# Kernel tuning notes

Measured on AMD Instinct MI355X. Metric: run time of the kernel, lower is better.

## Reference

```python
import jax, jax.numpy as jnp
import numpy as np

B = 4096
D = 512
N_I = 1000000
N_T = 1000000
GAMMA = 0.8
EPS = 1e-10
RHO_I = 8.0
RHO_T = 8.0
ETA_INIT = 1e-05
BETA_U = 0.5
GRAD_CLIP = 5.0
TAU_MIN, TAU_MAX = 0.005, 0.05
TAU_INIT = 0.01


def setup_inputs() -> dict:
    key = jax.random.key(0)
    k1, k2 = jax.random.split(key)
    img = jax.random.normal(k1, (B, D), jnp.float32)
    txt = jax.random.normal(k2, (B, D), jnp.float32)
    # CLIP-style L2-normalized features
    img = img / jnp.linalg.norm(img, axis=1, keepdims=True)
    txt = txt / jnp.linalg.norm(txt, axis=1, keepdims=True)
    return {
        "image_features": img,
        "text_features": txt,
        "s_I": jnp.zeros(N_I, jnp.float32),
        "s_T": jnp.zeros(N_T, jnp.float32),
        "b_I": jnp.zeros(N_I, jnp.float32),
        "b_T": jnp.zeros(N_T, jnp.float32),
        "u_I": jnp.zeros(N_I, jnp.float32),
        "u_T": jnp.zeros(N_T, jnp.float32),
        "tau_I": jnp.full((N_I,), TAU_INIT, jnp.float32),
        "tau_T": jnp.full((N_T,), TAU_INIT, jnp.float32),
        "image_ids": jnp.arange(B, dtype=jnp.int32),
        "text_ids": jnp.arange(B, dtype=jnp.int32),
        "epoch": 1,
    }


def reference(image_features, text_features, s_I, s_T, b_I, b_T, u_I, u_T,
              tau_I, tau_T, image_ids, text_ids, epoch):
    sg = jax.lax.stop_gradient
    sim = jnp.einsum('id,jd->ij', image_features, text_features)  # [B,B]
    diag = jnp.diagonal(sim)
    Bn = sim.shape[0]
    tau_img = tau_I[image_ids]  # [B]
    tau_txt = tau_T[text_ids]   # [B]
    image_diffs = sim - diag[:, None]
    text_diffs = sim - diag[None, :]
    # .detach() in the original -> stop_gradient here
    idt = sg(image_diffs / tau_img[:, None])
    tdt = sg(text_diffs / tau_txt[None, :])
    old_b_I = b_I[image_ids]
    old_b_T = b_T[text_ids]
    # running max for log-sum-exp stabilization
    b_I_row = jnp.maximum(idt.max(axis=1), old_b_I)
    b_T_col = jnp.maximum(tdt.max(axis=0), old_b_T)
    b_I_new = b_I.at[image_ids].set(b_I_row)
    b_T_new = b_T.at[text_ids].set(b_T_col)
    mask = 1.0 - jnp.eye(Bn, dtype=sim.dtype)
    exp_i = jnp.exp(idt - b_I_row[:, None]) * mask
    exp_t = jnp.exp(tdt - b_T_col[None, :]) * mask
    g_I = exp_i.sum(axis=1)
    g_T = exp_t.sum(axis=0)
    if epoch == 0:
        sI = g_I
        sT = g_T
    else:
        sI = (1.0 - GAMMA) * s_I[image_ids] * jnp.exp(old_b_I - b_I_row) + GAMMA * g_I
        sT = (1.0 - GAMMA) * s_T[text_ids] * jnp.exp(old_b_T - b_T_col) + GAMMA * g_T
    s_I_new = s_I.at[image_ids].set(sI)
    s_T_new = s_T.at[text_ids].set(sT)
    w_i = sg(exp_i / (sI[:, None] + EPS))
    w_t = sg(exp_t / (sT[None, :] + EPS))
    image_loss = (w_i * image_diffs).sum(axis=1)
    text_loss = (w_t * text_diffs).sum(axis=0)
    total_loss = image_loss.mean() + text_loss.mean()
    tw_i = jnp.log(sI / (Bn - 1)) + b_I_row + RHO_I - (w_i * idt).sum(axis=1)
    tw_t = jnp.log(sT / (Bn - 1)) + b_T_col + RHO_T - (w_t * tdt).sum(axis=0)
    # torch uses in-place clamp_ on a view, so the returned means are clipped
    tw_i = jnp.clip(tw_i, -GRAD_CLIP, GRAD_CLIP)
    tw_t = jnp.clip(tw_t, -GRAD_CLIP, GRAD_CLIP)
    u_I_val = (1.0 - BETA_U) * u_I[image_ids] + BETA_U * tw_i
    u_T_val = (1.0 - BETA_U) * u_T[text_ids] + BETA_U * tw_t
    u_I_new = u_I.at[image_ids].set(u_I_val)
    u_T_new = u_T.at[text_ids].set(u_T_val)
    tau_I_new = tau_I.at[image_ids].set(jnp.clip(tau_img - ETA_INIT * u_I_val, TAU_MIN, TAU_MAX))
    tau_T_new = tau_T.at[text_ids].set(jnp.clip(tau_txt - ETA_INIT * u_T_val, TAU_MIN, TAU_MAX))
    return (total_loss, tau_img.mean(), tau_txt.mean(), tw_i.mean(), tw_t.mean(),
            s_I_new, s_T_new, b_I_new, b_T_new, u_I_new, u_T_new, tau_I_new, tau_T_new)
```

## Files before the change

kernel.cpp:

```cpp
#include <hip/hip_runtime.h>

typedef unsigned short u16;
typedef unsigned int u32;

typedef __bf16 bf16x8 __attribute__((ext_vector_type(8)));
typedef float floatx4 __attribute__((ext_vector_type(4)));

__device__ __forceinline__ u16 f2bf(float f) {
    union { float f; u32 u; } c; c.f = f;
    u32 u = c.u;
    u32 r = u + 0x7FFFu + ((u >> 16) & 1u);
    return (u16)(r >> 16);
}
__device__ __forceinline__ float bf2f(u16 x) {
    union { u32 u; float f; } c; c.u = ((u32)x) << 16; return c.f;
}

__device__ __forceinline__ void comb(float& M, float& P0, float& P1,
                                     float m, float p0, float p1) {
    float nm = fmaxf(M, m);
    float s = __expf(M - nm), t = __expf(m - nm);
    P0 = P0 * s + p0 * t;
    P1 = P1 * s + p1 * t;
    M = nm;
}

__device__ __forceinline__ void gload16(const void* g, void* l) {
    __builtin_amdgcn_global_load_lds(
        (const __attribute__((address_space(1))) void*)g,
        (__attribute__((address_space(3))) void*)l, 16, 0, 0);
}

__global__ __launch_bounds__(256) void presplit(
    const float* __restrict__ a, const float* __restrict__ b,
    u16* __restrict__ Ah, u16* __restrict__ Al,
    u16* __restrict__ Bh, u16* __restrict__ Bl, int n,
    const float* __restrict__ tauI, const float* __restrict__ tauT,
    const int* __restrict__ img_ids, const int* __restrict__ txt_ids,
    float* __restrict__ taur, float* __restrict__ tauc,
    u32* __restrict__ ctrl) {
    if (blockIdx.y == 0 && blockIdx.x == 0 && threadIdx.x < 8)
        ctrl[threadIdx.x] = 0u;
    if (blockIdx.y == 0 && blockIdx.x < 16) {
        int t = blockIdx.x * 256 + threadIdx.x;
        taur[t] = tauI[img_ids[t]];
        tauc[t] = tauT[txt_ids[t]];
    }
    const float* src = blockIdx.y ? b : a;
    u16* dh = blockIdx.y ? Bh : Ah;
    u16* dl = blockIdx.y ? Bl : Al;
    int i = (blockIdx.x * 256 + threadIdx.x) * 8;
    if (i >= n) return;
    float4 v0 = *(const float4*)&src[i];
    float4 v1 = *(const float4*)&src[i + 4];
    float xs[8] = {v0.x, v0.y, v0.z, v0.w, v1.x, v1.y, v1.z, v1.w};
    u16 h[8], l[8];
#pragma unroll
    for (int e = 0; e < 8; e++) {
        h[e] = f2bf(xs[e]);
        l[e] = f2bf(xs[e] - bf2f(h[e]));
    }
    int r = i >> 9, k = i & 511;
    int off = (((r >> 4) << 4) + (k >> 5)) * 512 + ((((k >> 3) & 3) << 4) + (r & 15)) * 8;
    *(uint4*)&dh[off] = *(uint4*)h;
    *(uint4*)&dl[off] = *(uint4*)l;
}

__global__ __launch_bounds__(512, 2) void gemm_flash(
    const u16* __restrict__ Ah, const u16* __restrict__ Al,
    const u16* __restrict__ Bh, const u16* __restrict__ Bl,
    const float* __restrict__ taur, const float* __restrict__ tauc,
    float* __restrict__ rowpart, float* __restrict__ colpart,
    float* __restrict__ diag,
    const float* __restrict__ p0, const float* __restrict__ p1,
    const float* __restrict__ p2, const float* __restrict__ p3,
    const float* __restrict__ p4, const float* __restrict__ p5,
    const float* __restrict__ p6, const float* __restrict__ p7,
    float* __restrict__ out, long long n) {
    __shared__ u16 tiles[65536];

    const int bid  = blockIdx.x;
    const int tid  = threadIdx.x;
    const int wave = tid >> 6, lane = tid & 63;
    const int lr = lane & 15, quad = lane >> 4;
    const int waveM = wave >> 2, waveN = wave & 3;
    const int x = bid & 7, s = bid >> 3;
    const int rowtile = (x >> 2) * 8 + (s >> 2);
    const int coltile = (x & 3) * 4 + (s & 3);
    const int rowBase = rowtile * 256;
    const int colBase = coltile * 256;

    const int sa = wave >> 1;
    const u16* gb = (sa == 0) ? Ah : (sa == 1) ? Al : (sa == 2) ? Bh : Bl;
    const int base16 = ((sa < 2) ? rowBase : colBase) >> 4;
    const int jb = (wave & 1) * 8;

#define STAGE(slice, bufb)                                                    \
    {                                                                         \
        _Pragma("unroll")                                                     \
        for (int j = 0; j < 8; j++) {                                         \
            size_t ge = ((size_t)(base16 + jb + j)) * 8192 +                  \
                        (size_t)(slice) * 512 + lane * 8;                     \
            gload16(gb + ge, &tiles[(bufb) + (wave * 8 + j) * 512]);          \
        }                                                                     \
    }

    floatx4 acc[8][4];
#pragma unroll
    for (int mi = 0; mi < 8; mi++)
#pragma unroll
        for (int ni = 0; ni < 4; ni++) acc[mi][ni] = (floatx4)0.0f;

    const int Gq = (int)((n - 3) >> 2);
    const int ni32 = (int)n;
    float* dst5 = out + 5;

    STAGE(0, 0)

    if (bid == 0 && tid < 32) {
        int arr = tid >> 2, j = tid & 3;
        const float* sp = (arr & 4) ? ((arr & 2) ? ((arr & 1) ? p7 : p6) : ((arr & 1) ? p5 : p4))
                                    : ((arr & 2) ? ((arr & 1) ? p3 : p2) : ((arr & 1) ? p1 : p0));
        float* dp = dst5 + (size_t)arr * (size_t)n;
        long long tail0 = 3 + 4 * (long long)Gq;
        if (j < 3) dp[j] = sp[j];
        else
            for (long long z = tail0; z < n; z++) dp[z] = sp[z];
    }
    __syncthreads();

#pragma unroll 1
    for (int t = 0; t < 16; t++) {
        const int cb = (t & 1) << 15;
        const int nb = cb ^ 32768;
        if (t < 15) STAGE(t + 1, nb)

        bool docopy = false;
        float c0 = 0.f, c1 = 0.f, c2 = 0.f, c3 = 0.f;
        int cdst = 0;
        {
            int c = bid * 512 + tid + t * 131072;
            int ck = c >> 18;
            int g = c & 262143;
            if (g < Gq) {
                docopy = true;
                int ce = 3 + 4 * g;
                cdst = ck * ni32 + ce;
                const float* sp = (ck & 4) ? ((ck & 2) ? ((ck & 1) ? p7 : p6) : ((ck & 1) ? p5 : p4))
                                           : ((ck & 2) ? ((ck & 1) ? p3 : p2) : ((ck & 1) ? p1 : p0));
                c0 = sp[ce]; c1 = sp[ce + 1]; c2 = sp[ce + 2]; c3 = sp[ce + 3];
            }
        }

        {
            const int ab = cb + lane * 8;
            bf16x8 bh[4], bl[4];
#pragma unroll
            for (int ni = 0; ni < 4; ni++) {
                bh[ni] = *(const bf16x8*)&tiles[ab + (32 + waveN * 4 + ni) * 512];
                bl[ni] = *(const bf16x8*)&tiles[ab + (48 + waveN * 4 + ni) * 512];
            }
#pragma unroll
            for (int mi = 0; mi < 8; mi++) {
                bf16x8 ah = *(const bf16x8*)&tiles[ab + (waveM * 8 + mi) * 512];
                bf16x8 al = *(const bf16x8*)&tiles[ab + (16 + waveM * 8 + mi) * 512];
#pragma unroll
                for (int ni = 0; ni < 4; ni++) {
                    acc[mi][ni] = __builtin_amdgcn_mfma_f32_16x16x32_bf16(ah, bh[ni], acc[mi][ni], 0, 0, 0);
                    acc[mi][ni] = __builtin_amdgcn_mfma_f32_16x16x32_bf16(ah, bl[ni], acc[mi][ni], 0, 0, 0);
                    acc[mi][ni] = __builtin_amdgcn_mfma_f32_16x16x32_bf16(al, bh[ni], acc[mi][ni], 0, 0, 0);
                }
            }
        }

        if (docopy) {
            float4 q = {c0, c1, c2, c3};
            *(float4*)&dst5[cdst] = q;
        }
        __syncthreads();
    }
#undef STAGE

    float* redbuf = (float*)tiles;

    if (rowtile == coltile) {
#pragma unroll
        for (int mi = 0; mi < 8; mi++)
#pragma unroll
            for (int ni = 0; ni < 4; ni++) {
                if (waveM * 128 + mi * 16 != waveN * 64 + ni * 16) continue;
#pragma unroll
                for (int r = 0; r < 4; r++)
                    if (lr == quad * 4 + r)
                        diag[colBase + waveN * 64 + ni * 16 + lr] = acc[mi][ni][r];
            }
    }

#pragma unroll
    for (int mi = 0; mi < 8; mi++) {
#pragma unroll
        for (int r = 0; r < 4; r++) {
            int row_local = waveM * 128 + mi * 16 + quad * 4 + r;
            float vmax = fmaxf(fmaxf(acc[mi][0][r], acc[mi][1][r]),
                               fmaxf(acc[mi][2][r], acc[mi][3][r]));
#pragma unroll
            for (int mask = 1; mask <= 8; mask <<= 1)
                vmax = fmaxf(vmax, __shfl_xor(vmax, mask));
            float it = 1.0f / taur[rowBase + row_local];
            float M = vmax * it;
            float P0 = 0.f, P1 = 0.f;
#pragma unroll
            for (int ni = 0; ni < 4; ni++) {
                float y = acc[mi][ni][r] * it;
                float e = __expf(y - M);
                P0 += e;
                P1 += y * e;
            }
#pragma unroll
            for (int mask = 1; mask <= 8; mask <<= 1) {
                P0 += __shfl_xor(P0, mask);
                P1 += __shfl_xor(P1, mask);
            }
            if (lr == 0) {
                int xx = (row_local * 4 + waveN) * 3;
                redbuf[xx] = M; redbuf[xx + 1] = P0; redbuf[xx + 2] = P1;
            }
        }
    }

#pragma unroll
    for (int ni = 0; ni < 4; ni++) {
        int col_local = waveN * 64 + ni * 16 + lr;
        float vmax = -3.4e38f;
#pragma unroll
        for (int mi = 0; mi < 8; mi++)
            vmax = fmaxf(vmax,
                fmaxf(fmaxf(acc[mi][ni][0], acc[mi][ni][1]),
                      fmaxf(acc[mi][ni][2], acc[mi][ni][3])));
#pragma unroll
        for (int mask = 16; mask <= 32; mask <<= 1)
            vmax = fmaxf(vmax, __shfl_xor(vmax, mask));
        float it = 1.0f / tauc[colBase + col_local];
        float M = vmax * it;
        float P0 = 0.f, P1 = 0.f;
#pragma unroll
        for (int mi = 0; mi < 8; mi++)
#pragma unroll
            for (int r = 0; r < 4; r++) {
                float y = acc[mi][ni][r] * it;
                float e = __expf(y - M);
                P0 += e;
                P1 += y * e;
            }
#pragma unroll
        for (int mask = 16; mask <= 32; mask <<= 1) {
            P0 += __shfl_xor(P0, mask);
            P1 += __shfl_xor(P1, mask);
        }
        if (quad == 0) {
            int xx = 3072 + (col_local * 2 + waveM) * 3;
            redbuf[xx] = M; redbuf[xx + 1] = P0; redbuf[xx + 2] = P1;
        }
    }
    __syncthreads();

    if (tid < 256) {
        int xx = tid * 12;
        float M = redbuf[xx], P0 = redbuf[xx + 1], P1 = redbuf[xx + 2];
        comb(M, P0, P1, redbuf[xx + 3], redbuf[xx + 4], redbuf[xx + 5]);
        comb(M, P0, P1, redbuf[xx + 6], redbuf[xx + 7], redbuf[xx + 8]);
        comb(M, P0, P1, redbuf[xx + 9], redbuf[xx + 10], redbuf[xx + 11]);
        float* dst = &rowpart[(size_t)(rowBase + tid) * 48 + coltile * 3];
        dst[0] = M; dst[1] = P0; dst[2] = P1;
    } else {
        int c = tid - 256;
        int xx = 3072 + c * 6;
        float M = redbuf[xx], P0 = redbuf[xx + 1], P1 = redbuf[xx + 2];
        comb(M, P0, P1, redbuf[xx + 3], redbuf[xx + 4], redbuf[xx + 5]);
        float* dst = &colpart[(size_t)(colBase + c) * 48 + rowtile * 3];
        dst[0] = M; dst[1] = P0; dst[2] = P1;
    }
}

struct FinArgs {
    const float* rowpart; const float* colpart; const float* diag;
    const float* tauI; const float* sI; const float* bI; const float* uI;
    const float* tauT; const float* sT; const float* bT; const float* uT;
    const int* img_ids; const int* txt_ids; const int* epoch_p;
    float* out; u32* ctrl; long long n;
};

__global__ __launch_bounds__(256) void rows_final(FinArgs a) {
    int t = blockIdx.x * 256 + threadIdx.x;
    int side = t >> 12, i = t & 4095;
    const float* part   = side ? a.colpart : a.rowpart;
    const int*   ids    = side ? a.txt_ids : a.img_ids;
    const float* tau_in = side ? a.tauT : a.tauI;
    const float* s_in   = side ? a.sT   : a.sI;
    const float* b_in   = side ? a.bT   : a.bI;
    const float* u_in   = side ? a.uT   : a.uI;

    const int id = ids[i];
    const float dg = a.diag[i];

    const float4* p4 = (const float4*)(part + (size_t)i * 48);
    float v[48];
#pragma unroll
    for (int k = 0; k < 12; k++) {
        float4 q = p4[k];
        v[4 * k]     = q.x;
        v[4 * k + 1] = q.y;
        v[4 * k + 2] = q.z;
        v[4 * k + 3] = q.w;
    }
    float M = -3.4e38f, P0 = 0.f, P1 = 0.f;
#pragma unroll
    for (int k = 0; k < 16; k++)
        comb(M, P0, P1, v[3 * k], v[3 * k + 1], v[3 * k + 2]);

    const float tau   = tau_in[id];
    const float old_b = b_in[id];
    const float old_s = s_in[id];
    const float old_u = u_in[id];
    const float y_ii  = dg / tau;

    float b_row = fmaxf(M - y_ii, old_b);
    float e  = expf(M - y_ii - b_row);
    float S0 = P0 * e - expf(-b_row);
    float S1 = (P1 - y_ii * P0) * e;

    float g = S0;
    float sI = (*a.epoch_p == 0) ? g
             : 0.2f * old_s * expf(old_b - b_row) + 0.8f * g;
    float denom = sI + 1e-10f;
    float wsum = S1 / denom;
    float lossr = tau * wsum;
    float tw = logf(sI * (1.0f / 4095.0f)) + b_row + 8.0f - wsum;
    tw = fminf(fmaxf(tw, -5.0f), 5.0f);
    float uval = 0.5f * old_u + 0.5f * tw;
    float taun = fminf(fmaxf(tau - 1e-5f * uval, 0.005f), 0.05f);

    float* sect = a.out + 5;
    sect[(size_t)(0 + side) * (size_t)a.n + id] = sI;
    sect[(size_t)(2 + side) * (size_t)a.n + id] = b_row;
    sect[(size_t)(4 + side) * (size_t)a.n + id] = uval;
    sect[(size_t)(6 + side) * (size_t)a.n + id] = taun;

    __shared__ float sred[4][3];
    const int lane = threadIdx.x & 63, wv = threadIdx.x >> 6;
    float r0 = lossr, r1 = tw, r2 = tau;
#pragma unroll
    for (int o = 32; o > 0; o >>= 1) {
        r0 += __shfl_xor(r0, o);
        r1 += __shfl_xor(r1, o);
        r2 += __shfl_xor(r2, o);
    }
    if (lane == 0) { sred[wv][0] = r0; sred[wv][1] = r1; sred[wv][2] = r2; }
    __syncthreads();
    if (threadIdx.x == 0) {
        float t0 = sred[0][0] + sred[1][0] + sred[2][0] + sred[3][0];
        float t1 = sred[0][1] + sred[1][1] + sred[2][1] + sred[3][1];
        float t2 = sred[0][2] + sred[1][2] + sred[2][2] + sred[3][2];
        float* accs = (float*)a.ctrl;
        __hip_atomic_fetch_add(&accs[side * 3 + 0], t0, __ATOMIC_RELAXED,
                               __HIP_MEMORY_SCOPE_AGENT);
        __hip_atomic_fetch_add(&accs[side * 3 + 1], t1, __ATOMIC_RELAXED,
                               __HIP_MEMORY_SCOPE_AGENT);
        __hip_atomic_fetch_add(&accs[side * 3 + 2], t2, __ATOMIC_RELAXED,
                               __HIP_MEMORY_SCOPE_AGENT);
        u32 tk = __hip_atomic_fetch_add(&a.ctrl[6], 1u, __ATOMIC_ACQ_REL,
                                        __HIP_MEMORY_SCOPE_AGENT);
        if (tk == 31u) {
            float s0 = __hip_atomic_fetch_add(&accs[0], 0.0f, __ATOMIC_RELAXED, __HIP_MEMORY_SCOPE_AGENT);
            float s1 = __hip_atomic_fetch_add(&accs[1], 0.0f, __ATOMIC_RELAXED, __HIP_MEMORY_SCOPE_AGENT);
            float s2 = __hip_atomic_fetch_add(&accs[2], 0.0f, __ATOMIC_RELAXED, __HIP_MEMORY_SCOPE_AGENT);
            float s3 = __hip_atomic_fetch_add(&accs[3], 0.0f, __ATOMIC_RELAXED, __HIP_MEMORY_SCOPE_AGENT);
            float s4 = __hip_atomic_fetch_add(&accs[4], 0.0f, __ATOMIC_RELAXED, __HIP_MEMORY_SCOPE_AGENT);
            float s5 = __hip_atomic_fetch_add(&accs[5], 0.0f, __ATOMIC_RELAXED, __HIP_MEMORY_SCOPE_AGENT);
            const float inv = 1.0f / 4096.0f;
            a.out[0] = (s0 + s3) * inv;
            a.out[1] = s2 * inv;
            a.out[2] = s5 * inv;
            a.out[3] = s1 * inv;
            a.out[4] = s4 * inv;
        }
    }
}

extern "C" void kernel_launch(void* const* d_in, const int* in_sizes, int n_in,
                              void* d_out, int out_size, void* d_ws, size_t ws_size,
                              hipStream_t stream) {
    const float* img   = (const float*)d_in[0];
    const float* txt   = (const float*)d_in[1];
    const float* s_I   = (const float*)d_in[2];
    const float* s_T   = (const float*)d_in[3];
    const float* b_I   = (const float*)d_in[4];
    const float* b_T   = (const float*)d_in[5];
    const float* u_I   = (const float*)d_in[6];
    const float* u_T   = (const float*)d_in[7];
    const float* tau_I = (const float*)d_in[8];
    const float* tau_T = (const float*)d_in[9];
    const int* image_ids = (const int*)d_in[10];
    const int* text_ids  = (const int*)d_in[11];
    const int* epoch     = (const int*)d_in[12];
    float* out = (float*)d_out;
    const long long n = in_sizes[2];
    const int nfeat = in_sizes[0];

    const size_t MB = 1024 * 1024;
    u16* Ah = (u16*)d_ws;
    u16* Al = Ah + (size_t)nfeat;
    u16* Bh = Al + (size_t)nfeat;
    u16* Bl = Bh + (size_t)nfeat;
    float* rowpart = (float*)((char*)d_ws + 16 * MB);
    float* colpart = (float*)((char*)d_ws + 18 * MB);
    float* diag    = (float*)((char*)d_ws + 20 * MB);
    float* taur    = (float*)((char*)d_ws + 20 * MB + 256 * 1024);
    float* tauc    = (float*)((char*)d_ws + 20 * MB + 512 * 1024);
    u32*   ctrl    = (u32*)((char*)d_ws + 22 * MB);

    presplit<<<dim3((nfeat / 8 + 255) / 256, 2), 256, 0, stream>>>(
        img, txt, Ah, Al, Bh, Bl, nfeat,
        tau_I, tau_T, image_ids, text_ids, taur, tauc, ctrl);

    gemm_flash<<<256, 512, 0, stream>>>(
        Ah, Al, Bh, Bl, taur, tauc, rowpart, colpart, diag,
        s_I, s_T, b_I, b_T, u_I, u_T, tau_I, tau_T, out, n);

    FinArgs fa;
    fa.rowpart = rowpart; fa.colpart = colpart; fa.diag = diag;
    fa.tauI = tau_I; fa.sI = s_I; fa.bI = b_I; fa.uI = u_I;
    fa.tauT = tau_T; fa.sT = s_T; fa.bT = b_T; fa.uT = u_T;
    fa.img_ids = image_ids; fa.txt_ids = text_ids; fa.epoch_p = epoch;
    fa.out = out; fa.ctrl = ctrl; fa.n = n;
    rows_final<<<32, 256, 0, stream>>>(fa);
}
```

Baseline: 173.1 us.

## Halve GEMM column tile to 128, single-buffer LDS, double grid occupancy

The fused split-bf16 GEMM + flash-style reduction now uses 256x128 output tiles with 512 blocks, a single 48 KB shared buffer instead of a 128 KB double buffer, and launch bounds allowing 4 blocks per CU. The goal is to fill more CUs and raise occupancy so latency is hidden by other resident blocks instead of by explicit double buffering. The parameter-copy work is re-split across the larger grid, and row partials grow from 16 to 32 entries per row, so the final kernel is adjusted to match. Risks: less operand reuse per tile, a sync per K-slice with no prefetch, and possible register spilling under the tighter launch bound.

```diff
diff --git a/kernel.cpp b/kernel.cpp
--- a/kernel.cpp
+++ b/kernel.cpp
@@ -66,7 +66,7 @@
     *(uint4*)&dl[off] = *(uint4*)l;
 }
 
-__global__ __launch_bounds__(512, 2) void gemm_flash(
+__global__ __launch_bounds__(512, 4) void gemm_flash(
     const u16* __restrict__ Ah, const u16* __restrict__ Al,
     const u16* __restrict__ Bh, const u16* __restrict__ Bl,
     const float* __restrict__ taur, const float* __restrict__ tauc,
@@ -77,45 +77,47 @@
     const float* __restrict__ p4, const float* __restrict__ p5,
     const float* __restrict__ p6, const float* __restrict__ p7,
     float* __restrict__ out, long long n) {
-    __shared__ u16 tiles[65536];
+    __shared__ u16 tiles[24576];
 
     const int bid  = blockIdx.x;
     const int tid  = threadIdx.x;
     const int wave = tid >> 6, lane = tid & 63;
     const int lr = lane & 15, quad = lane >> 4;
-    const int waveM = wave >> 2, waveN = wave & 3;
+    const int waveM = wave >> 1, waveN = wave & 1;
     const int x = bid & 7, s = bid >> 3;
-    const int rowtile = (x >> 2) * 8 + (s >> 2);
-    const int coltile = (x & 3) * 4 + (s & 3);
+    const int rowtile = (x >> 2) * 8 + (s >> 3);
+    const int coltile = (x & 3) * 8 + (s & 7);
     const int rowBase = rowtile * 256;
-    const int colBase = coltile * 256;
-
-    const int sa = wave >> 1;
-    const u16* gb = (sa == 0) ? Ah : (sa == 1) ? Al : (sa == 2) ? Bh : Bl;
-    const int base16 = ((sa < 2) ? rowBase : colBase) >> 4;
-    const int jb = (wave & 1) * 8;
-
-#define STAGE(slice, bufb)                                                    \
+    const int colBase = coltile * 128;
+    const int rowBase16 = rowBase >> 4, colBase16 = colBase >> 4;
+    const size_t la = (size_t)(lane * 8);
+
+#define STAGE(slice)                                                          \
     {                                                                         \
-        _Pragma("unroll")                                                     \
-        for (int j = 0; j < 8; j++) {                                         \
-            size_t ge = ((size_t)(base16 + jb + j)) * 8192 +                  \
-                        (size_t)(slice) * 512 + lane * 8;                     \
-            gload16(gb + ge, &tiles[(bufb) + (wave * 8 + j) * 512]);          \
-        }                                                                     \
-    }
-
-    floatx4 acc[8][4];
-#pragma unroll
-    for (int mi = 0; mi < 8; mi++)
+        const size_t so = (size_t)(slice) * 512 + la;                         \
+        gload16(Ah + ((size_t)(rowBase16 + wave)) * 8192 + so,                \
+                &tiles[(wave) * 512]);                                        \
+        gload16(Ah + ((size_t)(rowBase16 + wave + 8)) * 8192 + so,            \
+                &tiles[(wave + 8) * 512]);                                    \
+        gload16(Al + ((size_t)(rowBase16 + wave)) * 8192 + so,                \
+                &tiles[(16 + wave) * 512]);                                   \
+        gload16(Al + ((size_t)(rowBase16 + wave + 8)) * 8192 + so,            \
+                &tiles[(24 + wave) * 512]);                                   \
+        gload16(Bh + ((size_t)(colBase16 + wave)) * 8192 + so,                \
+                &tiles[(32 + wave) * 512]);                                   \
+        gload16(Bl + ((size_t)(colBase16 + wave)) * 8192 + so,                \
+                &tiles[(40 + wave) * 512]);                                   \
+    }
+
+    floatx4 acc[4][4];
+#pragma unroll
+    for (int mi = 0; mi < 4; mi++)
 #pragma unroll
         for (int ni = 0; ni < 4; ni++) acc[mi][ni] = (floatx4)0.0f;
 
     const int Gq = (int)((n - 3) >> 2);
     const int ni32 = (int)n;
     float* dst5 = out + 5;
-
-    STAGE(0, 0)
 
     if (bid == 0 && tid < 32) {
         int arr = tid >> 2, j = tid & 3;
@@ -127,43 +129,39 @@
         else
             for (long long z = tail0; z < n; z++) dp[z] = sp[z];
     }
-    __syncthreads();
+
+    const int cg = bid * 512 + tid;
+    const int ab = (int)la;
 
 #pragma unroll 1
     for (int t = 0; t < 16; t++) {
-        const int cb = (t & 1) << 15;
-        const int nb = cb ^ 32768;
-        if (t < 15) STAGE(t + 1, nb)
+        STAGE(t)
 
         bool docopy = false;
         float c0 = 0.f, c1 = 0.f, c2 = 0.f, c3 = 0.f;
         int cdst = 0;
+        if (t < 8 && cg < Gq) {
+            docopy = true;
+            int ce = 3 + 4 * cg;
+            cdst = t * ni32 + ce;
+            const float* sp = (t & 4) ? ((t & 2) ? ((t & 1) ? p7 : p6) : ((t & 1) ? p5 : p4))
+                                      : ((t & 2) ? ((t & 1) ? p3 : p2) : ((t & 1) ? p1 : p0));
+            c0 = sp[ce]; c1 = sp[ce + 1]; c2 = sp[ce + 2]; c3 = sp[ce + 3];
+        }
+
+        __syncthreads();
+
         {
-            int c = bid * 512 + tid + t * 131072;
-            int ck = c >> 18;
-            int g = c & 262143;
-            if (g < Gq) {
-                docopy = true;
-                int ce = 3 + 4 * g;
-                cdst = ck * ni32 + ce;
-                const float* sp = (ck & 4) ? ((ck & 2) ? ((ck & 1) ? p7 : p6) : ((ck & 1) ? p5 : p4))
-                                           : ((ck & 2) ? ((ck & 1) ? p3 : p2) : ((ck & 1) ? p1 : p0));
-                c0 = sp[ce]; c1 = sp[ce + 1]; c2 = sp[ce + 2]; c3 = sp[ce + 3];
-            }
-        }
-
-        {
-            const int ab = cb + lane * 8;
             bf16x8 bh[4], bl[4];
 #pragma unroll
             for (int ni = 0; ni < 4; ni++) {
                 bh[ni] = *(const bf16x8*)&tiles[ab + (32 + waveN * 4 + ni) * 512];
-                bl[ni] = *(const bf16x8*)&tiles[ab + (48 + waveN * 4 + ni) * 512];
-            }
-#pragma unroll
-            for (int mi = 0; mi < 8; mi++) {
-                bf16x8 ah = *(const bf16x8*)&tiles[ab + (waveM * 8 + mi) * 512];
-                bf16x8 al = *(const bf16x8*)&tiles[ab + (16 + waveM * 8 + mi) * 512];
+                bl[ni] = *(const bf16x8*)&tiles[ab + (40 + waveN * 4 + ni) * 512];
+            }
+#pragma unroll
+            for (int mi = 0; mi < 4; mi++) {
+                bf16x8 ah = *(const bf16x8*)&tiles[ab + (waveM * 4 + mi) * 512];
+                bf16x8 al = *(const bf16x8*)&tiles[ab + (16 + waveM * 4 + mi) * 512];
 #pragma unroll
                 for (int ni = 0; ni < 4; ni++) {
                     acc[mi][ni] = __builtin_amdgcn_mfma_f32_16x16x32_bf16(ah, bh[ni], acc[mi][ni], 0, 0, 0);
@@ -183,12 +181,13 @@
 
     float* redbuf = (float*)tiles;
 
-    if (rowtile == coltile) {
-#pragma unroll
-        for (int mi = 0; mi < 8; mi++)
+    if ((coltile >> 1) == rowtile) {
+#pragma unroll
+        for (int mi = 0; mi < 4; mi++)
 #pragma unroll
             for (int ni = 0; ni < 4; ni++) {
-                if (waveM * 128 + mi * 16 != waveN * 64 + ni * 16) continue;
+                if (waveM * 64 + mi * 16 !=
+                    (coltile & 1) * 128 + waveN * 64 + ni * 16) continue;
 #pragma unroll
                 for (int r = 0; r < 4; r++)
                     if (lr == quad * 4 + r)
@@ -197,10 +196,10 @@
     }
 
 #pragma unroll
-    for (int mi = 0; mi < 8; mi++) {
+    for (int mi = 0; mi < 4; mi++) {
 #pragma unroll
         for (int r = 0; r < 4; r++) {
-            int row_local = waveM * 128 + mi * 16 + quad * 4 + r;
+            int row_local = waveM * 64 + mi * 16 + quad * 4 + r;
             float vmax = fmaxf(fmaxf(acc[mi][0][r], acc[mi][1][r]),
                                fmaxf(acc[mi][2][r], acc[mi][3][r]));
 #pragma unroll
@@ -222,7 +221,7 @@
                 P1 += __shfl_xor(P1, mask);
             }
             if (lr == 0) {
-                int xx = (row_local * 4 + waveN) * 3;
+                int xx = (row_local * 2 + waveN) * 3;
                 redbuf[xx] = M; redbuf[xx + 1] = P0; redbuf[xx + 2] = P1;
             }
         }
@@ -233,7 +232,7 @@
         int col_local = waveN * 64 + ni * 16 + lr;
         float vmax = -3.4e38f;
 #pragma unroll
-        for (int mi = 0; mi < 8; mi++)
+        for (int mi = 0; mi < 4; mi++)
             vmax = fmaxf(vmax,
                 fmaxf(fmaxf(acc[mi][ni][0], acc[mi][ni][1]),
                       fmaxf(acc[mi][ni][2], acc[mi][ni][3])));
@@ -244,7 +243,7 @@
         float M = vmax * it;
         float P0 = 0.f, P1 = 0.f;
 #pragma unroll
-        for (int mi = 0; mi < 8; mi++)
+        for (int mi = 0; mi < 4; mi++)
 #pragma unroll
             for (int r = 0; r < 4; r++) {
                 float y = acc[mi][ni][r] * it;
@@ -258,25 +257,25 @@
             P1 += __shfl_xor(P1, mask);
         }
         if (quad == 0) {
-            int xx = 3072 + (col_local * 2 + waveM) * 3;
+            int xx = 1536 + (col_local * 4 + waveM) * 3;
             redbuf[xx] = M; redbuf[xx + 1] = P0; redbuf[xx + 2] = P1;
         }
     }
     __syncthreads();
 
     if (tid < 256) {
-        int xx = tid * 12;
+        int xx = tid * 6;
+        float M = redbuf[xx], P0 = redbuf[xx + 1], P1 = redbuf[xx + 2];
+        comb(M, P0, P1, redbuf[xx + 3], redbuf[xx + 4], redbuf[xx + 5]);
+        float* dst = &rowpart[(size_t)(rowBase + tid) * 96 + coltile * 3];
+        dst[0] = M; dst[1] = P0; dst[2] = P1;
+    } else if (tid < 384) {
+        int c = tid - 256;
+        int xx = 1536 + c * 12;
         float M = redbuf[xx], P0 = redbuf[xx + 1], P1 = redbuf[xx + 2];
         comb(M, P0, P1, redbuf[xx + 3], redbuf[xx + 4], redbuf[xx + 5]);
         comb(M, P0, P1, redbuf[xx + 6], redbuf[xx + 7], redbuf[xx + 8]);
         comb(M, P0, P1, redbuf[xx + 9], redbuf[xx + 10], redbuf[xx + 11]);
-        float* dst = &rowpart[(size_t)(rowBase + tid) * 48 + coltile * 3];
-        dst[0] = M; dst[1] = P0; dst[2] = P1;
-    } else {
-        int c = tid - 256;
-        int xx = 3072 + c * 6;
-        float M = redbuf[xx], P0 = redbuf[xx + 1], P1 = redbuf[xx + 2];
-        comb(M, P0, P1, redbuf[xx + 3], redbuf[xx + 4], redbuf[xx + 5]);
         float* dst = &colpart[(size_t)(colBase + c) * 48 + rowtile * 3];
         dst[0] = M; dst[1] = P0; dst[2] = P1;
     }
@@ -293,7 +292,6 @@
 __global__ __launch_bounds__(256) void rows_final(FinArgs a) {
     int t = blockIdx.x * 256 + threadIdx.x;
     int side = t >> 12, i = t & 4095;
-    const float* part   = side ? a.colpart : a.rowpart;
     const int*   ids    = side ? a.txt_ids : a.img_ids;
     const float* tau_in = side ? a.tauT : a.tauI;
     const float* s_in   = side ? a.sT   : a.sI;
@@ -303,20 +301,36 @@
     const int id = ids[i];
     const float dg = a.diag[i];
 
-    const float4* p4 = (const float4*)(part + (size_t)i * 48);
-    float v[48];
-#pragma unroll
-    for (int k = 0; k < 12; k++) {
-        float4 q = p4[k];
-        v[4 * k]     = q.x;
-        v[4 * k + 1] = q.y;
-        v[4 * k + 2] = q.z;
-        v[4 * k + 3] = q.w;
-    }
     float M = -3.4e38f, P0 = 0.f, P1 = 0.f;
-#pragma unroll
-    for (int k = 0; k < 16; k++)
-        comb(M, P0, P1, v[3 * k], v[3 * k + 1], v[3 * k + 2]);
+    if (side == 0) {
+        const float4* p4 = (const float4*)(a.rowpart + (size_t)i * 96);
+        float v[96];
+#pragma unroll
+        for (int k = 0; k < 24; k++) {
+            float4 q = p4[k];
+            v[4 * k]     = q.x;
+            v[4 * k + 1] = q.y;
+            v[4 * k + 2] = q.z;
+            v[4 * k + 3] = q.w;
+        }
+#pragma unroll
+        for (int k = 0; k < 32; k++)
+            comb(M, P0, P1, v[3 * k], v[3 * k + 1], v[3 * k + 2]);
+    } else {
+        const float4* p4 = (const float4*)(a.colpart + (size_t)i * 48);
+        float v[48];
+#pragma unroll
+        for (int k = 0; k < 12; k++) {
+            float4 q = p4[k];
+            v[4 * k]     = q.x;
+            v[4 * k + 1] = q.y;
+            v[4 * k + 2] = q.z;
+            v[4 * k + 3] = q.w;
+        }
+#pragma unroll
+        for (int k = 0; k < 16; k++)
+            comb(M, P0, P1, v[3 * k], v[3 * k + 1], v[3 * k + 2]);
+    }
 
     const float tau   = tau_in[id];
     const float old_b = b_in[id];
@@ -423,7 +437,7 @@
         img, txt, Ah, Al, Bh, Bl, nfeat,
         tau_I, tau_T, image_ids, text_ids, taur, tauc, ctrl);
 
-    gemm_flash<<<256, 512, 0, stream>>>(
+    gemm_flash<<<512, 512, 0, stream>>>(
         Ah, Al, Bh, Bl, taur, tauc, rowpart, colpart, diag,
         s_I, s_T, b_I, b_T, u_I, u_T, tau_I, tau_T, out, n);
 
```

New measurement: 183.4 us. 6.0% more time.
